# Optimization experiments

Measured on AMD Instinct MI355X. Metric: run time of the kernel, lower is better.

## Reference

```python
import jax, jax.numpy as jnp
import numpy as np
from functools import reduce

N_QUBITS = 12
DIM = 2 ** N_QUBITS  # 4096
BATCH = 512
TWO_PI = 6.283185307179586


def u3_gate(t):
    # Standard U3(theta, phi, lam) single-qubit gate, complex64 2x2.
    th, ph, la = t[0], t[1], t[2]
    c = jnp.cos(th * 0.5).astype(jnp.complex64)
    s = jnp.sin(th * 0.5).astype(jnp.complex64)
    e_la = jnp.exp(1j * la.astype(jnp.complex64))
    e_ph = jnp.exp(1j * ph.astype(jnp.complex64))
    row0 = jnp.stack([c, -e_la * s])
    row1 = jnp.stack([e_ph * s, e_ph * e_la * c])
    return jnp.stack([row0, row1])  # [2,2] complex64


def full_unitary(thetas):
    # Kron product of per-qubit U3 gates -> [2^n, 2^n] complex64,
    # matching U3(*self.thetas) in the original layer.
    gates = [u3_gate(thetas[i]) for i in range(N_QUBITS)]
    return reduce(jnp.kron, gates)


def setup_inputs() -> dict:
    key = jax.random.key(0)
    k1, k2, k3 = jax.random.split(key, 3)
    thetas = jax.random.uniform(k1, (N_QUBITS, 3), dtype=jnp.float32) * TWO_PI
    state_re = jax.random.normal(k2, (BATCH, DIM, 1), dtype=jnp.float32)
    state_im = jax.random.normal(k3, (BATCH, DIM, 1), dtype=jnp.float32)
    return {"thetas": thetas, "state_re": state_re, "state_im": state_im}


def reference(thetas, state_re, state_im):
    U = full_unitary(thetas)                      # [DIM, DIM] complex64
    state = state_re.astype(jnp.complex64) + 1j * state_im.astype(jnp.complex64)
    out = jnp.einsum('ij,bjk->bik', U, state)     # matrix @ inputs, batched
    # Complex output expressed as real/imag concat on last axis: [B, DIM, 2]
    return jnp.concatenate([out.real, out.imag], axis=-1)
```

## Files before the change

kernel.cpp:

```cpp
#include <hip/hip_runtime.h>
#include <math.h>

#define NQ    12
#define DIM   4096
#define BATCH 512

typedef float nt_f2 __attribute__((ext_vector_type(2)));

#define PAD2(i) ((i) + 2 * ((i) >> 4))

#define LEVEL(q, J) do {                                                    \
    const float4 GA = *(const float4*)&g[q][0];                             \
    const float4 GB = *(const float4*)&g[q][4];                             \
    _Pragma("unroll")                                                       \
    for (int p = 0; p < 8; ++p) {                                           \
        const int r0 = ((p >> (J)) << ((J) + 1)) | (p & ((1 << (J)) - 1));  \
        const int r1 = r0 | (1 << (J));                                     \
        const float ar = x[r0].x, ai = x[r0].y;                             \
        const float br = x[r1].x, bi = x[r1].y;                             \
        x[r0].x = GA.x * ar - GA.y * ai + GA.z * br - GA.w * bi;            \
        x[r0].y = GA.x * ai + GA.y * ar + GA.z * bi + GA.w * br;            \
        x[r1].x = GB.x * ar - GB.y * ai + GB.z * br - GB.w * bi;            \
        x[r1].y = GB.x * ai + GB.y * ar + GB.z * bi + GB.w * br;            \
    }                                                                       \
} while (0)

__global__ __launch_bounds__(256) void u3_apply_kernel(
    const float* __restrict__ thetas,
    const float* __restrict__ sre,
    const float* __restrict__ sim_,
    float*       __restrict__ out)
{
    __shared__ __align__(16) float2 L[4608];
    __shared__ __align__(16) float  g[NQ][8];

    const int b = blockIdx.x;
    const int t = threadIdx.x;

    const float4* pre = (const float4*)(sre  + (size_t)b * DIM) + 4 * t;
    const float4* pim = (const float4*)(sim_ + (size_t)b * DIM) + 4 * t;
    float4 vr0 = pre[0], vr1 = pre[1], vr2 = pre[2], vr3 = pre[3];
    float4 vi0 = pim[0], vi1 = pim[1], vi2 = pim[2], vi3 = pim[3];

    if (t < NQ) {
        float th = thetas[t * 3 + 0];
        float ph = thetas[t * 3 + 1];
        float la = thetas[t * 3 + 2];
        float c, s, cl, sl, cp, sp;
        __sincosf(th * 0.5f, &s, &c);
        __sincosf(la, &sl, &cl);
        __sincosf(ph, &sp, &cp);
        g[t][0] = c;        g[t][1] = 0.0f;
        g[t][2] = -cl * s;  g[t][3] = -sl * s;
        g[t][4] = cp * s;   g[t][5] = sp * s;
        g[t][6] = (cp * cl - sp * sl) * c;
        g[t][7] = (sp * cl + cp * sl) * c;
    }
    __syncthreads();

    float2 x[16];
    x[ 0] = make_float2(vr0.x, vi0.x); x[ 1] = make_float2(vr0.y, vi0.y);
    x[ 2] = make_float2(vr0.z, vi0.z); x[ 3] = make_float2(vr0.w, vi0.w);
    x[ 4] = make_float2(vr1.x, vi1.x); x[ 5] = make_float2(vr1.y, vi1.y);
    x[ 6] = make_float2(vr1.z, vi1.z); x[ 7] = make_float2(vr1.w, vi1.w);
    x[ 8] = make_float2(vr2.x, vi2.x); x[ 9] = make_float2(vr2.y, vi2.y);
    x[10] = make_float2(vr2.z, vi2.z); x[11] = make_float2(vr2.w, vi2.w);
    x[12] = make_float2(vr3.x, vi3.x); x[13] = make_float2(vr3.y, vi3.y);
    x[14] = make_float2(vr3.z, vi3.z); x[15] = make_float2(vr3.w, vi3.w);

    LEVEL(11, 0); LEVEL(10, 1); LEVEL(9, 2); LEVEL(8, 3);

#pragma unroll
    for (int k = 0; k < 8; ++k) {
        *(float4*)&L[PAD2((t << 4) | (2 * k))] =
            make_float4(x[2 * k].x, x[2 * k].y, x[2 * k + 1].x, x[2 * k + 1].y);
    }
    __syncthreads();
    {
        const int base = ((t & 0xF0) << 4) | (t & 15);
#pragma unroll
        for (int r = 0; r < 16; ++r) x[r] = L[PAD2(base | (r << 4))];
    }

    LEVEL(7, 0); LEVEL(6, 1); LEVEL(5, 2); LEVEL(4, 3);

    {
        const int base = ((t & 0xF0) << 4) | (t & 15);
#pragma unroll
        for (int r = 0; r < 16; ++r) L[PAD2(base | (r << 4))] = x[r];
    }
    __syncthreads();
#pragma unroll
    for (int r = 0; r < 16; ++r) x[r] = L[PAD2((r << 8) | t)];

    LEVEL(3, 0); LEVEL(2, 1); LEVEL(1, 2); LEVEL(0, 3);

    {
        float2* o2 = (float2*)out + (size_t)b * DIM;
#pragma unroll
        for (int r = 0; r < 16; ++r) {
            nt_f2 v; v.x = x[r].x; v.y = x[r].y;
            __builtin_nontemporal_store(v, (nt_f2*)&o2[(r << 8) | t]);
        }
    }
}

extern "C" void kernel_launch(void* const* d_in, const int* in_sizes, int n_in,
                              void* d_out, int out_size, void* d_ws, size_t ws_size,
                              hipStream_t stream) {
    const float* thetas = (const float*)d_in[0];
    const float* sre    = (const float*)d_in[1];
    const float* sim_   = (const float*)d_in[2];
    float* out = (float*)d_out;

    u3_apply_kernel<<<BATCH, 256, 0, stream>>>(thetas, sre, sim_, out);
}
```

Measured before the change: 16.16 us.

## Split each batch element's state across two blocks by top qubit

Each batch element is now handled by two 128-thread blocks, one per value of the most-significant qubit. Each block first applies qubit 0's gate row while loading both halves of the state, then runs the remaining 11 gate levels on its 2048-element half with half the shared memory. This doubles the block count to expose more parallelism and occupancy. The cost is that every input element is read twice from global memory, and the nontemporal output stores are replaced with ordinary stores.

```diff
diff --git a/kernel.cpp b/kernel.cpp
--- a/kernel.cpp
+++ b/kernel.cpp
@@ -3,9 +3,10 @@
 
 #define NQ    12
 #define DIM   4096
+#define HALF  2048
 #define BATCH 512
-
-typedef float nt_f2 __attribute__((ext_vector_type(2)));
+#define NBLK  1024
+#define NTHR  128
 
 #define PAD2(i) ((i) + 2 * ((i) >> 4))
 
@@ -25,22 +26,34 @@
     }                                                                       \
 } while (0)
 
-__global__ __launch_bounds__(256) void u3_apply_kernel(
+#define CMB1(lrc, lic, hrc, hic) make_float2(                               \
+    P.x * (lrc) - P.y * (lic) + P.z * (hrc) - P.w * (hic),                  \
+    P.x * (lic) + P.y * (lrc) + P.z * (hic) + P.w * (hrc))
+
+__global__ __launch_bounds__(NTHR) void u3_half_kernel(
     const float* __restrict__ thetas,
     const float* __restrict__ sre,
     const float* __restrict__ sim_,
     float*       __restrict__ out)
 {
-    __shared__ __align__(16) float2 L[4608];
+    __shared__ __align__(16) float2 L[2304];
     __shared__ __align__(16) float  g[NQ][8];
 
     const int b = blockIdx.x;
+    const int e = b >> 1;
+    const int h = b & 1;
     const int t = threadIdx.x;
 
-    const float4* pre = (const float4*)(sre  + (size_t)b * DIM) + 4 * t;
-    const float4* pim = (const float4*)(sim_ + (size_t)b * DIM) + 4 * t;
-    float4 vr0 = pre[0], vr1 = pre[1], vr2 = pre[2], vr3 = pre[3];
-    float4 vi0 = pim[0], vi1 = pim[1], vi2 = pim[2], vi3 = pim[3];
+    const float* Sr = sre  + (size_t)e * DIM;
+    const float* Si = sim_ + (size_t)e * DIM;
+    const float4* plr = (const float4*)Sr + 4 * t;
+    const float4* pli = (const float4*)Si + 4 * t;
+    const float4* phr = (const float4*)(Sr + HALF) + 4 * t;
+    const float4* phi = (const float4*)(Si + HALF) + 4 * t;
+    float4 lr0 = plr[0], lr1 = plr[1], lr2 = plr[2], lr3 = plr[3];
+    float4 li0 = pli[0], li1 = pli[1], li2 = pli[2], li3 = pli[3];
+    float4 hr0 = phr[0], hr1 = phr[1], hr2 = phr[2], hr3 = phr[3];
+    float4 hi0 = phi[0], hi1 = phi[1], hi2 = phi[2], hi3 = phi[3];
 
     if (t < NQ) {
         float th = thetas[t * 3 + 0];
@@ -58,15 +71,24 @@
     }
     __syncthreads();
 
+    const float4 P = *(const float4*)&g[0][4 * h];
     float2 x[16];
-    x[ 0] = make_float2(vr0.x, vi0.x); x[ 1] = make_float2(vr0.y, vi0.y);
-    x[ 2] = make_float2(vr0.z, vi0.z); x[ 3] = make_float2(vr0.w, vi0.w);
-    x[ 4] = make_float2(vr1.x, vi1.x); x[ 5] = make_float2(vr1.y, vi1.y);
-    x[ 6] = make_float2(vr1.z, vi1.z); x[ 7] = make_float2(vr1.w, vi1.w);
-    x[ 8] = make_float2(vr2.x, vi2.x); x[ 9] = make_float2(vr2.y, vi2.y);
-    x[10] = make_float2(vr2.z, vi2.z); x[11] = make_float2(vr2.w, vi2.w);
-    x[12] = make_float2(vr3.x, vi3.x); x[13] = make_float2(vr3.y, vi3.y);
-    x[14] = make_float2(vr3.z, vi3.z); x[15] = make_float2(vr3.w, vi3.w);
+    x[ 0] = CMB1(lr0.x, li0.x, hr0.x, hi0.x);
+    x[ 1] = CMB1(lr0.y, li0.y, hr0.y, hi0.y);
+    x[ 2] = CMB1(lr0.z, li0.z, hr0.z, hi0.z);
+    x[ 3] = CMB1(lr0.w, li0.w, hr0.w, hi0.w);
+    x[ 4] = CMB1(lr1.x, li1.x, hr1.x, hi1.x);
+    x[ 5] = CMB1(lr1.y, li1.y, hr1.y, hi1.y);
+    x[ 6] = CMB1(lr1.z, li1.z, hr1.z, hi1.z);
+    x[ 7] = CMB1(lr1.w, li1.w, hr1.w, hi1.w);
+    x[ 8] = CMB1(lr2.x, li2.x, hr2.x, hi2.x);
+    x[ 9] = CMB1(lr2.y, li2.y, hr2.y, hi2.y);
+    x[10] = CMB1(lr2.z, li2.z, hr2.z, hi2.z);
+    x[11] = CMB1(lr2.w, li2.w, hr2.w, hi2.w);
+    x[12] = CMB1(lr3.x, li3.x, hr3.x, hi3.x);
+    x[13] = CMB1(lr3.y, li3.y, hr3.y, hi3.y);
+    x[14] = CMB1(lr3.z, li3.z, hr3.z, hi3.z);
+    x[15] = CMB1(lr3.w, li3.w, hr3.w, hi3.w);
 
     LEVEL(11, 0); LEVEL(10, 1); LEVEL(9, 2); LEVEL(8, 3);
 
@@ -76,32 +98,24 @@
             make_float4(x[2 * k].x, x[2 * k].y, x[2 * k + 1].x, x[2 * k + 1].y);
     }
     __syncthreads();
-    {
-        const int base = ((t & 0xF0) << 4) | (t & 15);
+    const int base1 = ((t & 0x70) << 4) | (t & 15);
 #pragma unroll
-        for (int r = 0; r < 16; ++r) x[r] = L[PAD2(base | (r << 4))];
-    }
+    for (int r = 0; r < 16; ++r) x[r] = L[PAD2(base1 | (r << 4))];
 
     LEVEL(7, 0); LEVEL(6, 1); LEVEL(5, 2); LEVEL(4, 3);
 
-    {
-        const int base = ((t & 0xF0) << 4) | (t & 15);
 #pragma unroll
-        for (int r = 0; r < 16; ++r) L[PAD2(base | (r << 4))] = x[r];
-    }
+    for (int r = 0; r < 16; ++r) L[PAD2(base1 | (r << 4))] = x[r];
     __syncthreads();
 #pragma unroll
-    for (int r = 0; r < 16; ++r) x[r] = L[PAD2((r << 8) | t)];
+    for (int r = 0; r < 16; ++r) x[r] = L[PAD2((r << 7) | t)];
 
-    LEVEL(3, 0); LEVEL(2, 1); LEVEL(1, 2); LEVEL(0, 3);
+    LEVEL(3, 1); LEVEL(2, 2); LEVEL(1, 3);
 
     {
-        float2* o2 = (float2*)out + (size_t)b * DIM;
+        float2* o2 = (float2*)out + (size_t)e * DIM + (size_t)h * HALF;
 #pragma unroll
-        for (int r = 0; r < 16; ++r) {
-            nt_f2 v; v.x = x[r].x; v.y = x[r].y;
-            __builtin_nontemporal_store(v, (nt_f2*)&o2[(r << 8) | t]);
-        }
+        for (int r = 0; r < 16; ++r) o2[(r << 7) | t] = x[r];
     }
 }
 
@@ -113,5 +127,5 @@
     const float* sim_   = (const float*)d_in[2];
     float* out = (float*)d_out;
 
-    u3_apply_kernel<<<BATCH, 256, 0, stream>>>(thetas, sre, sim_, out);
+    u3_half_kernel<<<NBLK, NTHR, 0, stream>>>(thetas, sre, sim_, out);
 }
```

Measured after the change: 20.00 us. 23.8% more time.

## Process each batch element with a single wave holding 64 amplitudes per thread

Applied to the files above, without the earlier changes.

Restructures the kernel so one 64-thread wave handles a whole state vector. Each thread keeps 64 complex amplitudes in registers, which allows six qubit levels per pass and needs only one LDS transpose (with XOR swizzling, split real/imag arrays) instead of two padded transposes. The aim is to cut LDS round trips and block-wide barriers and to exploit the structure of the gate (g00 imaginary part is zero) to save FLOPs. It also drops the nontemporal stores. The costs are much higher register pressure (128 floats per thread) and reduced occupancy. Global loads become strided per thread (64 consecutive floats per thread) rather than coalesced across the wave.

```diff
diff --git a/kernel.cpp b/kernel.cpp
--- a/kernel.cpp
+++ b/kernel.cpp
@@ -5,42 +5,45 @@
 #define DIM   4096
 #define BATCH 512
 
-typedef float nt_f2 __attribute__((ext_vector_type(2)));
-
-#define PAD2(i) ((i) + 2 * ((i) >> 4))
-
 #define LEVEL(q, J) do {                                                    \
-    const float4 GA = *(const float4*)&g[q][0];                             \
-    const float4 GB = *(const float4*)&g[q][4];                             \
+    const float c    = g[q][0];                                             \
+    const float g01r = g[q][2], g01i = g[q][3];                             \
+    const float g10r = g[q][4], g10i = g[q][5];                             \
+    const float g11r = g[q][6], g11i = g[q][7];                             \
     _Pragma("unroll")                                                       \
-    for (int p = 0; p < 8; ++p) {                                           \
+    for (int p = 0; p < 32; ++p) {                                          \
         const int r0 = ((p >> (J)) << ((J) + 1)) | (p & ((1 << (J)) - 1));  \
         const int r1 = r0 | (1 << (J));                                     \
-        const float ar = x[r0].x, ai = x[r0].y;                             \
-        const float br = x[r1].x, bi = x[r1].y;                             \
-        x[r0].x = GA.x * ar - GA.y * ai + GA.z * br - GA.w * bi;            \
-        x[r0].y = GA.x * ai + GA.y * ar + GA.z * bi + GA.w * br;            \
-        x[r1].x = GB.x * ar - GB.y * ai + GB.z * br - GB.w * bi;            \
-        x[r1].y = GB.x * ai + GB.y * ar + GB.z * bi + GB.w * br;            \
+        const float ar = xr[r0], ai = xi[r0];                               \
+        const float br = xr[r1], bi = xi[r1];                               \
+        xr[r0] = c * ar + (g01r * br - g01i * bi);                          \
+        xi[r0] = c * ai + (g01r * bi + g01i * br);                          \
+        xr[r1] = (g10r * ar - g10i * ai) + (g11r * br - g11i * bi);         \
+        xi[r1] = (g10r * ai + g10i * ar) + (g11r * bi + g11i * br);         \
     }                                                                       \
 } while (0)
 
-__global__ __launch_bounds__(256) void u3_apply_kernel(
+__global__ __launch_bounds__(64) void u3_wave_kernel(
     const float* __restrict__ thetas,
     const float* __restrict__ sre,
     const float* __restrict__ sim_,
     float*       __restrict__ out)
 {
-    __shared__ __align__(16) float2 L[4608];
-    __shared__ __align__(16) float  g[NQ][8];
+    __shared__ float Lr[DIM];
+    __shared__ float Li[DIM];
+    __shared__ __align__(16) float g[NQ][8];
 
-    const int b = blockIdx.x;
+    const int e = blockIdx.x;
     const int t = threadIdx.x;
 
-    const float4* pre = (const float4*)(sre  + (size_t)b * DIM) + 4 * t;
-    const float4* pim = (const float4*)(sim_ + (size_t)b * DIM) + 4 * t;
-    float4 vr0 = pre[0], vr1 = pre[1], vr2 = pre[2], vr3 = pre[3];
-    float4 vi0 = pim[0], vi1 = pim[1], vi2 = pim[2], vi3 = pim[3];
+    const float4* pre = (const float4*)(sre  + (size_t)e * DIM + t * 64);
+    const float4* pim = (const float4*)(sim_ + (size_t)e * DIM + t * 64);
+    float xr[64], xi[64];
+#pragma unroll
+    for (int k = 0; k < 16; ++k) {
+        *(float4*)&xr[4 * k] = pre[k];
+        *(float4*)&xi[4 * k] = pim[k];
+    }
 
     if (t < NQ) {
         float th = thetas[t * 3 + 0];
@@ -58,50 +61,31 @@
     }
     __syncthreads();
 
-    float2 x[16];
-    x[ 0] = make_float2(vr0.x, vi0.x); x[ 1] = make_float2(vr0.y, vi0.y);
-    x[ 2] = make_float2(vr0.z, vi0.z); x[ 3] = make_float2(vr0.w, vi0.w);
-    x[ 4] = make_float2(vr1.x, vi1.x); x[ 5] = make_float2(vr1.y, vi1.y);
-    x[ 6] = make_float2(vr1.z, vi1.z); x[ 7] = make_float2(vr1.w, vi1.w);
-    x[ 8] = make_float2(vr2.x, vi2.x); x[ 9] = make_float2(vr2.y, vi2.y);
-    x[10] = make_float2(vr2.z, vi2.z); x[11] = make_float2(vr2.w, vi2.w);
-    x[12] = make_float2(vr3.x, vi3.x); x[13] = make_float2(vr3.y, vi3.y);
-    x[14] = make_float2(vr3.z, vi3.z); x[15] = make_float2(vr3.w, vi3.w);
-
-    LEVEL(11, 0); LEVEL(10, 1); LEVEL(9, 2); LEVEL(8, 3);
+    LEVEL(11, 0); LEVEL(10, 1); LEVEL(9, 2);
+    LEVEL(8, 3);  LEVEL(7, 4);  LEVEL(6, 5);
 
 #pragma unroll
-    for (int k = 0; k < 8; ++k) {
-        *(float4*)&L[PAD2((t << 4) | (2 * k))] =
-            make_float4(x[2 * k].x, x[2 * k].y, x[2 * k + 1].x, x[2 * k + 1].y);
-    }
-    __syncthreads();
-    {
-        const int base = ((t & 0xF0) << 4) | (t & 15);
-#pragma unroll
-        for (int r = 0; r < 16; ++r) x[r] = L[PAD2(base | (r << 4))];
-    }
-
-    LEVEL(7, 0); LEVEL(6, 1); LEVEL(5, 2); LEVEL(4, 3);
-
-    {
-        const int base = ((t & 0xF0) << 4) | (t & 15);
-#pragma unroll
-        for (int r = 0; r < 16; ++r) L[PAD2(base | (r << 4))] = x[r];
+    for (int r = 0; r < 64; ++r) {
+        const int a = (t << 6) | (r ^ t);
+        Lr[a] = xr[r];
+        Li[a] = xi[r];
     }
     __syncthreads();
 #pragma unroll
-    for (int r = 0; r < 16; ++r) x[r] = L[PAD2((r << 8) | t)];
+    for (int r = 0; r < 64; ++r) {
+        const int a = (r << 6) | (t ^ r);
+        xr[r] = Lr[a];
+        xi[r] = Li[a];
+    }
 
-    LEVEL(3, 0); LEVEL(2, 1); LEVEL(1, 2); LEVEL(0, 3);
+    LEVEL(5, 0); LEVEL(4, 1); LEVEL(3, 2);
+    LEVEL(2, 3); LEVEL(1, 4); LEVEL(0, 5);
 
     {
-        float2* o2 = (float2*)out + (size_t)b * DIM;
+        float2* o2 = (float2*)out + (size_t)e * DIM;
 #pragma unroll
-        for (int r = 0; r < 16; ++r) {
-            nt_f2 v; v.x = x[r].x; v.y = x[r].y;
-            __builtin_nontemporal_store(v, (nt_f2*)&o2[(r << 8) | t]);
-        }
+        for (int r = 0; r < 64; ++r)
+            o2[(r << 6) | t] = make_float2(xr[r], xi[r]);
     }
 }
 
@@ -113,5 +97,5 @@
     const float* sim_   = (const float*)d_in[2];
     float* out = (float*)d_out;
 
-    u3_apply_kernel<<<BATCH, 256, 0, stream>>>(thetas, sre, sim_, out);
+    u3_wave_kernel<<<BATCH, 64, 0, stream>>>(thetas, sre, sim_, out);
 }
```

After: 23.81 us. +47.3%, slower.

## Reassign qubit levels so global loads are coalesced across threads

Applied to the files above, without the earlier changes.

Each thread now loads four float4 values strided by 256 vectors, so a wavefront reads contiguous memory instead of each thread reading 64 contiguous bytes. The qubit-to-level assignment and the shared-memory transposes are rebuilt so the first stage handles bits 0,1,10,11, the second bits 6-9 and the third bits 2-5. Output stores change to plain stores with a 64-stride pattern, dropping the nontemporal hint. This risks different LDS bank conflicts and less coalesced output writes.

```diff
diff --git a/kernel.cpp b/kernel.cpp
--- a/kernel.cpp
+++ b/kernel.cpp
@@ -4,8 +4,6 @@
 #define NQ    12
 #define DIM   4096
 #define BATCH 512
-
-typedef float nt_f2 __attribute__((ext_vector_type(2)));
 
 #define PAD2(i) ((i) + 2 * ((i) >> 4))
 
@@ -37,10 +35,12 @@
     const int b = blockIdx.x;
     const int t = threadIdx.x;
 
-    const float4* pre = (const float4*)(sre  + (size_t)b * DIM) + 4 * t;
-    const float4* pim = (const float4*)(sim_ + (size_t)b * DIM) + 4 * t;
-    float4 vr0 = pre[0], vr1 = pre[1], vr2 = pre[2], vr3 = pre[3];
-    float4 vi0 = pim[0], vi1 = pim[1], vi2 = pim[2], vi3 = pim[3];
+    const float4* pre = (const float4*)(sre  + (size_t)b * DIM);
+    const float4* pim = (const float4*)(sim_ + (size_t)b * DIM);
+    float4 vr0 = pre[t],       vr1 = pre[256 + t],
+           vr2 = pre[512 + t], vr3 = pre[768 + t];
+    float4 vi0 = pim[t],       vi1 = pim[256 + t],
+           vi2 = pim[512 + t], vi3 = pim[768 + t];
 
     if (t < NQ) {
         float th = thetas[t * 3 + 0];
@@ -68,40 +68,38 @@
     x[12] = make_float2(vr3.x, vi3.x); x[13] = make_float2(vr3.y, vi3.y);
     x[14] = make_float2(vr3.z, vi3.z); x[15] = make_float2(vr3.w, vi3.w);
 
-    LEVEL(11, 0); LEVEL(10, 1); LEVEL(9, 2); LEVEL(8, 3);
+    LEVEL(11, 0); LEVEL(10, 1); LEVEL(1, 2); LEVEL(0, 3);
 
 #pragma unroll
-    for (int k = 0; k < 8; ++k) {
-        *(float4*)&L[PAD2((t << 4) | (2 * k))] =
-            make_float4(x[2 * k].x, x[2 * k].y, x[2 * k + 1].x, x[2 * k + 1].y);
+    for (int k = 0; k < 4; ++k) {
+        const int pa = PAD2((k << 10) | (t << 2));
+        *(float4*)&L[pa] =
+            make_float4(x[4 * k].x,     x[4 * k].y,
+                        x[4 * k + 1].x, x[4 * k + 1].y);
+        *(float4*)&L[pa + 2] =
+            make_float4(x[4 * k + 2].x, x[4 * k + 2].y,
+                        x[4 * k + 3].x, x[4 * k + 3].y);
     }
     __syncthreads();
-    {
-        const int base = ((t & 0xF0) << 4) | (t & 15);
+    const int base1 = ((t >> 2) << 6) | (t & 3);
 #pragma unroll
-        for (int r = 0; r < 16; ++r) x[r] = L[PAD2(base | (r << 4))];
-    }
+    for (int r = 0; r < 16; ++r) x[r] = L[PAD2(base1 | (r << 2))];
 
-    LEVEL(7, 0); LEVEL(6, 1); LEVEL(5, 2); LEVEL(4, 3);
+    LEVEL(9, 0); LEVEL(8, 1); LEVEL(7, 2); LEVEL(6, 3);
 
-    {
-        const int base = ((t & 0xF0) << 4) | (t & 15);
 #pragma unroll
-        for (int r = 0; r < 16; ++r) L[PAD2(base | (r << 4))] = x[r];
-    }
+    for (int r = 0; r < 16; ++r) L[PAD2(base1 | (r << 2))] = x[r];
     __syncthreads();
+    const int base2 = ((t >> 6) << 10) | (t & 63);
 #pragma unroll
-    for (int r = 0; r < 16; ++r) x[r] = L[PAD2((r << 8) | t)];
+    for (int r = 0; r < 16; ++r) x[r] = L[PAD2(base2 | (r << 6))];
 
-    LEVEL(3, 0); LEVEL(2, 1); LEVEL(1, 2); LEVEL(0, 3);
+    LEVEL(5, 0); LEVEL(4, 1); LEVEL(3, 2); LEVEL(2, 3);
 
     {
         float2* o2 = (float2*)out + (size_t)b * DIM;
 #pragma unroll
-        for (int r = 0; r < 16; ++r) {
-            nt_f2 v; v.x = x[r].x; v.y = x[r].y;
-            __builtin_nontemporal_store(v, (nt_f2*)&o2[(r << 8) | t]);
-        }
+        for (int r = 0; r < 16; ++r) o2[base2 | (r << 6)] = x[r];
     }
 }
 
```

Result: slower. 17.29 us (+6.9%).
